# Performance work log

Measured on AMD Instinct MI355X. Metric: run time of the kernel, lower is better.

## Reference

```python
import jax, jax.numpy as jnp
import numpy as np

N_EMBD = 2048
HIDDEN = 2 * N_EMBD        # 4096
ADAPT = HIDDEN // 16       # 256
B, S = 4, 2048


def _layernorm(x, g, b, eps=1e-5):
    mu = jnp.mean(x, axis=-1, keepdims=True)
    var = jnp.var(x, axis=-1, keepdims=True)
    return (x - mu) * jax.lax.rsqrt(var + eps) * g + b


def setup_inputs() -> dict:
    key = jax.random.key(0)
    ks = jax.random.split(key, 7)
    scale = 1.0 / np.sqrt(N_EMBD)
    adapt_scale = scale * 0.01
    return {
        "x": jax.random.normal(ks[0], (B, S, N_EMBD), dtype=jnp.float32),
        "W_up": jax.random.normal(ks[1], (HIDDEN, N_EMBD), dtype=jnp.float32) * scale,
        "W_gate": jax.random.normal(ks[2], (HIDDEN, N_EMBD), dtype=jnp.float32) * scale,
        "W_down": jax.random.normal(ks[3], (N_EMBD, HIDDEN), dtype=jnp.float32) * scale,
        "W_pre": jax.random.normal(ks[4], (ADAPT, N_EMBD), dtype=jnp.float32) * adapt_scale,
        "W_post": jax.random.normal(ks[5], (ADAPT, HIDDEN), dtype=jnp.float32) * adapt_scale,
        "W_proj": jax.random.normal(ks[6], (HIDDEN, ADAPT), dtype=jnp.float32) * adapt_scale,
        "ln_g": jnp.ones((ADAPT,), dtype=jnp.float32),
        "ln_b": jnp.zeros((ADAPT,), dtype=jnp.float32),
    }


def reference(x, W_up, W_gate, W_down, W_pre, W_post, W_proj, ln_g, ln_b):
    # SwiGLU trunk
    up = jnp.einsum('bsd,hd->bsh', x, W_up)
    gate = jnp.einsum('bsd,hd->bsh', x, W_gate)
    hidden = jax.nn.silu(gate) * up                      # [B,S,H]
    # Low-rank quadratic adapter
    adapt_in = _layernorm(jnp.einsum('bsd,ad->bsa', x, W_pre), ln_g, ln_b)       # [B,S,A]
    adapt_out = _layernorm(jnp.einsum('bsh,ah->bsa', hidden, W_post), ln_g, ln_b)  # [B,S,A]
    aw = jnp.einsum('bsa,bta->bst', adapt_in, adapt_out)  # [B,S,S]
    aw = jax.nn.silu(jnp.clip(aw, -5.0, 5.0))
    adapt = jnp.einsum('bst,bta->bsa', aw, adapt_in)      # [B,S,A]
    adapt = 0.1 * jnp.einsum('bsa,ha->bsh', adapt, W_proj)
    hidden = hidden + adapt
    out = jnp.einsum('bsh,dh->bsd', hidden, W_down)       # dropout p=0 -> identity
    return out
```

## Files before the change

### kernel.cpp

```cpp
#include <hip/hip_runtime.h>
#include <cstdint>
#include <cstddef>

typedef unsigned short u16;
typedef short short8 __attribute__((ext_vector_type(8)));
typedef float f32x4 __attribute__((ext_vector_type(4)));

__device__ __forceinline__ u16 f2bf(float f) {
  union { float f; unsigned u; } x; x.f = f;
  unsigned r = x.u + 0x7FFFu + ((x.u >> 16) & 1u);
  return (u16)(r >> 16);
}
__device__ __forceinline__ float b2f(u16 h) {
  union { unsigned u; float f; } x; x.u = ((unsigned)h) << 16;
  return x.f;
}
__device__ __forceinline__ float silu_f(float v) {
  return v / (1.f + __expf(-v));
}
__device__ __forceinline__ void gll(const u16* g, u16* l) {
  __builtin_amdgcn_global_load_lds((const __attribute__((address_space(1))) unsigned*)g,
                                   (__attribute__((address_space(3))) unsigned*)l, 16, 0, 0);
}

__global__ __launch_bounds__(256) void cvt_k(const float4* __restrict__ in,
                                             ushort4* __restrict__ out, int n4) {
  int i = blockIdx.x * 256 + threadIdx.x;
  if (i >= n4) return;
  float4 v = in[i];
  ushort4 o;
  o.x = f2bf(v.x); o.y = f2bf(v.y); o.z = f2bf(v.z); o.w = f2bf(v.w);
  out[i] = o;
}

__global__ __launch_bounds__(256) void red_ln_k(const float* __restrict__ part,
                                                const float* __restrict__ g,
                                                const float* __restrict__ b,
                                                u16* __restrict__ out,
                                                u16* __restrict__ outT, int Mtot) {
  const int row = blockIdx.x;
  const int a = threadIdx.x;
  const size_t stride = (size_t)Mtot * 256;
  const size_t base = (size_t)row * 256 + a;
  float v = part[base] + part[base + stride] + part[base + 2 * stride] + part[base + 3 * stride];
  float s = v, s2 = v * v;
#pragma unroll
  for (int o = 32; o; o >>= 1) { s += __shfl_down(s, o, 64); s2 += __shfl_down(s2, o, 64); }
  __shared__ float red[8];
  int l = a & 63, w = a >> 6;
  if (l == 0) { red[w] = s; red[4 + w] = s2; }
  __syncthreads();
  s  = red[0] + red[1] + red[2] + red[3];
  s2 = red[4] + red[5] + red[6] + red[7];
  float mu  = s * 0.00390625f;
  float var = s2 * 0.00390625f - mu * mu;
  float rs  = rsqrtf(var + 1e-5f);
  float o   = (v - mu) * rs * g[a] + b[a];
  u16 ob = f2bf(o);
  out[base] = ob;
  if (outT) {
    int bi = row >> 11, t = row & 2047;
    outT[((size_t)bi * 256 + a) * 2048 + t] = ob;
  }
}

__global__ __launch_bounds__(256) void red_k(const float* __restrict__ part,
                                             u16* __restrict__ out, int Mtot) {
  const int row = blockIdx.x;
  const int a = threadIdx.x;
  const size_t stride = (size_t)Mtot * 256;
  const size_t base = (size_t)row * 256 + a;
  float v = part[base] + part[base + stride] + part[base + 2 * stride] + part[base + 3 * stride];
  out[base] = f2bf(v);
}

template <int EPI>
__global__ __launch_bounds__(256) void gemm_bt(const u16* __restrict__ A,
                                               const u16* __restrict__ B,
                                               void* __restrict__ Cv,
                                               int M, int N, int K,
                                               long bA, long bB, long bC) {
  __shared__ u16 Al[128 * 64];
  __shared__ u16 Bl[128 * 64];
  const int tid  = threadIdx.x;
  const int bz   = blockIdx.z;
  const int brow = blockIdx.y * 128;
  const int bcol = blockIdx.x * 128;
  A += (size_t)bz * bA;
  B += (size_t)bz * bB;
  const int lane = tid & 63;
  const int w = tid >> 6, wr = w >> 1, wc = w & 1;
  const int srow = tid >> 3;
  const int scol = (tid & 7) * 8;

  f32x4 acc[4][4] = {};

  for (int kt = 0; kt < K; kt += 64) {
#pragma unroll
    for (int i = 0; i < 4; ++i)
      gll(A + (size_t)(brow + i * 32 + srow) * K + kt + scol, &Al[(i * 256 + tid) * 8]);
#pragma unroll
    for (int i = 0; i < 4; ++i)
      gll(B + (size_t)(bcol + i * 32 + srow) * K + kt + scol, &Bl[(i * 256 + tid) * 8]);
    __syncthreads();
#pragma unroll
    for (int kk = 0; kk < 2; ++kk) {
      short8 af[4], bfr[4];
      const int ko = kk * 32 + (lane >> 4) * 8;
#pragma unroll
      for (int m = 0; m < 4; ++m)
        af[m] = *(const short8*)&Al[(wr * 64 + m * 16 + (lane & 15)) * 64 + ko];
#pragma unroll
      for (int n = 0; n < 4; ++n)
        bfr[n] = *(const short8*)&Bl[(wc * 64 + n * 16 + (lane & 15)) * 64 + ko];
#pragma unroll
      for (int m = 0; m < 4; ++m)
#pragma unroll
        for (int n = 0; n < 4; ++n)
          acc[m][n] = __builtin_amdgcn_mfma_f32_16x16x32_bf16(af[m], bfr[n], acc[m][n], 0, 0, 0);
    }
    __syncthreads();
  }

  const int col0 = bcol + wc * 64 + (lane & 15);
  const int row0 = brow + wr * 64 + ((lane >> 4) << 2);
  u16* Cb = (u16*)Cv + (size_t)bz * bC;
#pragma unroll
  for (int m = 0; m < 4; ++m)
#pragma unroll
    for (int j = 0; j < 4; ++j) {
      size_t roff = (size_t)(row0 + m * 16 + j) * N + col0;
#pragma unroll
      for (int n = 0; n < 4; ++n) {
        float v = acc[m][n][j];
        if (EPI == 2) {
          v = fminf(5.f, fmaxf(-5.f, v));
          v = silu_f(v);
        }
        Cb[roff + n * 16] = f2bf(v);
      }
    }
}

__global__ __launch_bounds__(256) void gemm_sk(const u16* __restrict__ A,
                                               const u16* __restrict__ B,
                                               float* __restrict__ part,
                                               int M, int N, int Kfull, int Kc,
                                               long bA, long bB, int Mtot) {
  const int z  = blockIdx.z;
  const int b  = z >> 2, sk = z & 3;
  const int brow = blockIdx.y * 128;
  const int bcol = blockIdx.x * 128;
  A += (size_t)b * bA + (size_t)sk * Kc;
  B += (size_t)b * bB + (size_t)sk * Kc;

  __shared__ u16 Al[128 * 64];
  __shared__ u16 Bl[128 * 64];
  const int tid  = threadIdx.x;
  const int lane = tid & 63;
  const int w = tid >> 6, wr = w >> 1, wc = w & 1;
  const int srow = tid >> 3;
  const int scol = (tid & 7) * 8;

  f32x4 acc[4][4] = {};

  for (int kt = 0; kt < Kc; kt += 64) {
#pragma unroll
    for (int i = 0; i < 4; ++i)
      gll(A + (size_t)(brow + i * 32 + srow) * Kfull + kt + scol, &Al[(i * 256 + tid) * 8]);
#pragma unroll
    for (int i = 0; i < 4; ++i)
      gll(B + (size_t)(bcol + i * 32 + srow) * Kfull + kt + scol, &Bl[(i * 256 + tid) * 8]);
    __syncthreads();
#pragma unroll
    for (int kk = 0; kk < 2; ++kk) {
      short8 af[4], bfr[4];
      const int ko = kk * 32 + (lane >> 4) * 8;
#pragma unroll
      for (int m = 0; m < 4; ++m)
        af[m] = *(const short8*)&Al[(wr * 64 + m * 16 + (lane & 15)) * 64 + ko];
#pragma unroll
      for (int n = 0; n < 4; ++n)
        bfr[n] = *(const short8*)&Bl[(wc * 64 + n * 16 + (lane & 15)) * 64 + ko];
#pragma unroll
      for (int m = 0; m < 4; ++m)
#pragma unroll
        for (int n = 0; n < 4; ++n)
          acc[m][n] = __builtin_amdgcn_mfma_f32_16x16x32_bf16(af[m], bfr[n], acc[m][n], 0, 0, 0);
    }
    __syncthreads();
  }

  const int col0 = bcol + wc * 64 + (lane & 15);
  const int row0 = brow + wr * 64 + ((lane >> 4) << 2);
  float* P = part + ((size_t)sk * Mtot + (size_t)b * M) * N;
#pragma unroll
  for (int m = 0; m < 4; ++m)
#pragma unroll
    for (int j = 0; j < 4; ++j) {
      size_t roff = (size_t)(row0 + m * 16 + j) * N + col0;
#pragma unroll
      for (int n = 0; n < 4; ++n) P[roff + n * 16] = acc[m][n][j];
    }
}

template <int EPI>
__global__ __launch_bounds__(512, 2) void gemm256(const u16* __restrict__ A,
                                                  const u16* __restrict__ B,
                                                  void* __restrict__ Cv,
                                                  const u16* __restrict__ H,
                                                  int M, int N, int K,
                                                  long bA, long bB, long bC) {
  __shared__ __align__(16) u16 As[32768];
  __shared__ __align__(16) u16 Bs[32768];

  const int tid = threadIdx.x;
  const int bz  = blockIdx.z;
  A += (size_t)bz * bA;
  B += (size_t)bz * bB;

  const int gx = gridDim.x;
  const int nwg = gx * gridDim.y;
  int orig = blockIdx.y * gx + blockIdx.x;
  {
    int q = nwg >> 3, r = nwg & 7;
    int xcd = orig & 7, idx = orig >> 3;
    orig = (xcd < r) ? xcd * (q + 1) + idx : r * (q + 1) + (xcd - r) * q + idx;
  }
  const int brow = (orig / gx) * 256;
  const int bcol = (orig % gx) * 256;

  const int lane = tid & 63;
  const int wid  = tid >> 6;
  const int wm = wid >> 2, wn = wid & 3;

  const int srow = tid >> 3;
  const int scol = ((((tid & 7) << 4) ^ ((srow & 7) << 4)) >> 1);
  const u16* Abase = A + (size_t)(brow + srow) * K + scol;
  const u16* Bbase = B + (size_t)(bcol + srow) * K + scol;

  const int fr  = lane & 15;
  const int cs0 = ((((lane >> 4) << 4) ^ ((lane & 7) << 4)) >> 1);
  const int cs1 = cs0 ^ 32;
  const int bro = (wn & 1) * 64;

  const int NT = K >> 6;

  f32x4 acc[8][4] = {};

  {
#pragma unroll
    for (int h = 0; h < 2; ++h) {
      const u16* s = Abase + (size_t)(h * 128) * K;
      u16* d = &As[h * 8192 + tid * 8];
      gll(s, d); gll(s + (size_t)64 * K, d + 4096);
    }
#pragma unroll
    for (int h = 0; h < 2; ++h) {
      const u16* s = Bbase + (size_t)(h * 128) * K;
      u16* d = &Bs[h * 8192 + tid * 8];
      gll(s, d); gll(s + (size_t)64 * K, d + 4096);
    }
  }
  asm volatile("s_waitcnt vmcnt(0)" ::: "memory");
  __builtin_amdgcn_s_barrier();

  for (int t = 0; t < NT; ++t) {
    const int cur = t & 1, nxt = cur ^ 1;
    const bool pf = (t + 1 < NT);
    const int ktn = (t + 1) << 6;
    const u16* aH = &As[(cur * 2 + wm) * 8192];
    const u16* bH = &Bs[(cur * 2 + (wn >> 1)) * 8192];
    short8 af[4], bf[4];

#pragma unroll
    for (int m = 0; m < 4; ++m) af[m] = *(const short8*)(aH + (m * 16 + fr) * 64 + cs0);
#pragma unroll
    for (int n = 0; n < 4; ++n) bf[n] = *(const short8*)(bH + (bro + n * 16 + fr) * 64 + cs0);
    if (pf) {
#pragma unroll
      for (int h = 0; h < 2; ++h) {
        const u16* s = Abase + (size_t)(h * 128) * K + ktn;
        u16* d = &As[(nxt * 2 + h) * 8192 + tid * 8];
        gll(s, d); gll(s + (size_t)64 * K, d + 4096);
      }
    }
    __builtin_amdgcn_s_barrier();
    asm volatile("s_waitcnt lgkmcnt(0)" ::: "memory");
    __builtin_amdgcn_s_setprio(1);
#pragma unroll
    for (int m = 0; m < 4; ++m)
#pragma unroll
      for (int n = 0; n < 4; ++n)
        acc[m][n] = __builtin_amdgcn_mfma_f32_16x16x32_bf16(af[m], bf[n], acc[m][n], 0, 0, 0);
    __builtin_amdgcn_s_setprio(0);
    __builtin_amdgcn_s_barrier();

#pragma unroll
    for (int m = 0; m < 4; ++m) af[m] = *(const short8*)(aH + (64 + m * 16 + fr) * 64 + cs0);
    if (pf) {
#pragma unroll
      for (int h = 0; h < 2; ++h) {
        const u16* s = Bbase + (size_t)(h * 128) * K + ktn;
        u16* d = &Bs[(nxt * 2 + h) * 8192 + tid * 8];
        gll(s, d); gll(s + (size_t)64 * K, d + 4096);
      }
    }
    __builtin_amdgcn_s_barrier();
    asm volatile("s_waitcnt lgkmcnt(0)" ::: "memory");
    __builtin_amdgcn_s_setprio(1);
#pragma unroll
    for (int m = 0; m < 4; ++m)
#pragma unroll
      for (int n = 0; n < 4; ++n)
        acc[4 + m][n] = __builtin_amdgcn_mfma_f32_16x16x32_bf16(af[m], bf[n], acc[4 + m][n], 0, 0, 0);
    __builtin_amdgcn_s_setprio(0);
    __builtin_amdgcn_s_barrier();

#pragma unroll
    for (int m = 0; m < 4; ++m) af[m] = *(const short8*)(aH + (m * 16 + fr) * 64 + cs1);
#pragma unroll
    for (int n = 0; n < 4; ++n) bf[n] = *(const short8*)(bH + (bro + n * 16 + fr) * 64 + cs1);
    __builtin_amdgcn_s_barrier();
    asm volatile("s_waitcnt lgkmcnt(0)" ::: "memory");
    __builtin_amdgcn_s_setprio(1);
#pragma unroll
    for (int m = 0; m < 4; ++m)
#pragma unroll
      for (int n = 0; n < 4; ++n)
        acc[m][n] = __builtin_amdgcn_mfma_f32_16x16x32_bf16(af[m], bf[n], acc[m][n], 0, 0, 0);
    __builtin_amdgcn_s_setprio(0);
    __builtin_amdgcn_s_barrier();

#pragma unroll
    for (int m = 0; m < 4; ++m) af[m] = *(const short8*)(aH + (64 + m * 16 + fr) * 64 + cs1);
    __builtin_amdgcn_s_barrier();
    asm volatile("s_waitcnt lgkmcnt(0)" ::: "memory");
    __builtin_amdgcn_s_setprio(1);
#pragma unroll
    for (int m = 0; m < 4; ++m)
#pragma unroll
      for (int n = 0; n < 4; ++n)
        acc[4 + m][n] = __builtin_amdgcn_mfma_f32_16x16x32_bf16(af[m], bf[n], acc[4 + m][n], 0, 0, 0);
    __builtin_amdgcn_s_setprio(0);
    asm volatile("s_waitcnt vmcnt(0)" ::: "memory");
    __builtin_amdgcn_s_barrier();
  }

  const int col0 = bcol + wn * 64 + fr;
  const int row0 = brow + wm * 128 + ((lane >> 4) << 2);

  if (EPI == 0) {
    float* Cf = (float*)Cv + (size_t)bz * bC;
#pragma unroll
    for (int m = 0; m < 8; ++m)
#pragma unroll
      for (int j = 0; j < 4; ++j) {
        size_t roff = (size_t)(row0 + m * 16 + j) * N + col0;
#pragma unroll
        for (int n = 0; n < 4; ++n) Cf[roff + n * 16] = acc[m][n][j];
      }
  } else if (EPI == 1) {
    u16* Cb = (u16*)Cv + (size_t)bz * bC;
#pragma unroll
    for (int m = 0; m < 8; ++m)
#pragma unroll
      for (int j = 0; j < 4; ++j) {
        size_t roff = (size_t)(row0 + m * 16 + j) * N + col0;
#pragma unroll
        for (int n = 0; n < 4; ++n) Cb[roff + n * 16] = f2bf(acc[m][n][j]);
      }
  } else if (EPI == 2) {
    u16* Cb = (u16*)Cv + (size_t)bz * bC;
#pragma unroll
    for (int m = 0; m < 8; ++m)
#pragma unroll
      for (int j = 0; j < 4; ++j) {
        size_t roff = (size_t)(row0 + m * 16 + j) * N + col0;
#pragma unroll
        for (int n = 0; n < 4; ++n) {
          float v = acc[m][n][j];
          v = fminf(5.f, fmaxf(-5.f, v));
          Cb[roff + n * 16] = f2bf(silu_f(v));
        }
      }
  } else if (EPI == 3) {
    u16* Cb = (u16*)Cv + (size_t)bz * bC;
    const u16* Hb = H + (size_t)bz * bC;
#pragma unroll
    for (int m = 0; m < 8; ++m)
#pragma unroll
      for (int j = 0; j < 4; ++j) {
        size_t roff = (size_t)(row0 + m * 16 + j) * N + col0;
#pragma unroll
        for (int n = 0; n < 4; ++n) {
          size_t idx = roff + n * 16;
          Cb[idx] = f2bf(b2f(Hb[idx]) + 0.1f * acc[m][n][j]);
        }
      }
  } else {
    u16* Cb = (u16*)Cv + (size_t)bz * bC;
    const u16* Hb = H + (size_t)bz * bC;
#pragma unroll
    for (int m = 0; m < 8; ++m)
#pragma unroll
      for (int j = 0; j < 4; ++j) {
        size_t roff = (size_t)(row0 + m * 16 + j) * N + col0;
#pragma unroll
        for (int n = 0; n < 4; ++n) {
          size_t idx = roff + n * 16;
          Cb[idx] = f2bf(silu_f(acc[m][n][j]) * b2f(Hb[idx]));
        }
      }
  }
}

extern "C" void kernel_launch(void* const* d_in, const int* in_sizes, int n_in,
                              void* d_out, int out_size, void* d_ws, size_t ws_size,
                              hipStream_t stream) {
  const float* x      = (const float*)d_in[0];
  const float* W_up   = (const float*)d_in[1];
  const float* W_gate = (const float*)d_in[2];
  const float* W_down = (const float*)d_in[3];
  const float* W_pre  = (const float*)d_in[4];
  const float* W_post = (const float*)d_in[5];
  const float* W_proj = (const float*)d_in[6];
  const float* ln_g   = (const float*)d_in[7];
  const float* ln_b   = (const float*)d_in[8];
  (void)in_sizes; (void)n_in; (void)out_size; (void)ws_size;

  const int D = 2048, Hh = 4096, A_ = 256, Bn = 4, S = 2048, M = 8192;

  char* p = (char*)d_ws;
  u16* xb      = (u16*)p; p += (size_t)M * D * 2;
  u16* Wup_b   = (u16*)p; p += (size_t)Hh * D * 2;
  u16* Wgate_b = (u16*)p; p += (size_t)Hh * D * 2;
  u16* Wdown_b = (u16*)p; p += (size_t)D * Hh * 2;
  u16* Wpre_b  = (u16*)p; p += (size_t)A_ * D * 2;
  u16* Wpost_b = (u16*)p; p += (size_t)A_ * Hh * 2;
  u16* Wproj_b = (u16*)p; p += (size_t)Hh * A_ * 2;
  u16* hidden  = (u16*)p; p += (size_t)M * Hh * 2;
  u16* scratch = (u16*)p; p += (size_t)M * Hh * 2;
  char* q = (char*)scratch;
  u16*   aw        = (u16*)q; q += (size_t)Bn * S * S * 2;
  u16*   adapt_in  = (u16*)q; q += (size_t)M * A_ * 2;
  u16*   adapt_inT = (u16*)q; q += (size_t)M * A_ * 2;
  u16*   adapt_out = (u16*)q; q += (size_t)M * A_ * 2;
  u16*   adaptb    = (u16*)q; q += (size_t)M * A_ * 2;
  float* part = (float*)Wup_b;

  auto cvt = [&](const float* src, u16* dst, size_t n) {
    int n4 = (int)(n / 4);
    cvt_k<<<dim3((n4 + 255) / 256), dim3(256), 0, stream>>>((const float4*)src, (ushort4*)dst, n4);
  };
  cvt(x,      xb,      (size_t)M * D);
  cvt(W_up,   Wup_b,   (size_t)Hh * D);
  cvt(W_gate, Wgate_b, (size_t)Hh * D);
  cvt(W_down, Wdown_b, (size_t)D * Hh);
  cvt(W_pre,  Wpre_b,  (size_t)A_ * D);
  cvt(W_post, Wpost_b, (size_t)A_ * Hh);
  cvt(W_proj, Wproj_b, (size_t)Hh * A_);

  gemm256<1><<<dim3(Hh / 256, M / 256, 1), 512, 0, stream>>>(xb, Wup_b, hidden, nullptr,
                                                             M, Hh, D, 0, 0, 0);
  gemm256<4><<<dim3(Hh / 256, M / 256, 1), 512, 0, stream>>>(xb, Wgate_b, hidden, hidden,
                                                             M, Hh, D, 0, 0, 0);

  gemm_sk<<<dim3(A_ / 128, M / 128, 4), 256, 0, stream>>>(xb, Wpre_b, part,
                                                          M, A_, D, D / 4, 0, 0, M);
  red_ln_k<<<dim3(M), 256, 0, stream>>>(part, ln_g, ln_b, adapt_in, adapt_inT, M);

  gemm_sk<<<dim3(A_ / 128, M / 128, 4), 256, 0, stream>>>(hidden, Wpost_b, part,
                                                          M, A_, Hh, Hh / 4, 0, 0, M);
  red_ln_k<<<dim3(M), 256, 0, stream>>>(part, ln_g, ln_b, adapt_out, nullptr, M);

  gemm_bt<2><<<dim3(S / 128, S / 128, Bn), 256, 0, stream>>>(adapt_in, adapt_out, aw,
                                                             S, S, A_,
                                                             (long)S * A_, (long)S * A_, (long)S * S);

  gemm_sk<<<dim3(A_ / 128, S / 128, Bn * 4), 256, 0, stream>>>(aw, adapt_inT, part,
                                                               S, A_, S, S / 4,
                                                               (long)S * S, (long)A_ * S, M);
  red_k<<<dim3(M), 256, 0, stream>>>(part, adaptb, M);

  gemm256<3><<<dim3(Hh / 256, M / 256, 1), 512, 0, stream>>>(adaptb, Wproj_b, hidden, hidden,
                                                             M, Hh, A_, 0, 0, 0);

  gemm256<0><<<dim3(D / 256, M / 256, 1), 512, 0, stream>>>(hidden, Wdown_b, d_out, nullptr,
                                                            M, D, Hh, 0, 0, 0);
}
```

Baseline: 622.6 us.

## Split gemm256 K-tiles into half-stages with deeper prefetch; fuse seven conversion launches

The 256x256 GEMM now stores each 64-wide K tile as two 32-wide halves with a new XOR swizzle. Loads for the next half-tiles are issued one to two phases ahead, with partial vmcnt waits instead of a full drain each iteration, and the last tiles are handled in a separate tail loop. This aims to hide global-to-LDS latency behind the MFMA work. Separately, the seven fp32-to-bf16 conversion kernels are merged into one launch over the contiguous workspace, using hardcoded offsets that only fit these shapes.

```diff
diff --git a/kernel.cpp b/kernel.cpp
--- a/kernel.cpp
+++ b/kernel.cpp
@@ -23,14 +23,31 @@
                                    (__attribute__((address_space(3))) unsigned*)l, 16, 0, 0);
 }
 
-__global__ __launch_bounds__(256) void cvt_k(const float4* __restrict__ in,
-                                             ushort4* __restrict__ out, int n4) {
-  int i = blockIdx.x * 256 + threadIdx.x;
-  if (i >= n4) return;
-  float4 v = in[i];
+__global__ __launch_bounds__(256) void cvt7_k(const float4* __restrict__ s0,
+                                              const float4* __restrict__ s1,
+                                              const float4* __restrict__ s2,
+                                              const float4* __restrict__ s3,
+                                              const float4* __restrict__ s4,
+                                              const float4* __restrict__ s5,
+                                              const float4* __restrict__ s6,
+                                              ushort4* __restrict__ dst) {
+  const int i = blockIdx.x * 256 + threadIdx.x;
+  const int o1 = 4194304, o2 = 6291456, o3 = 8388608, o4 = 10485760,
+            o5 = 10616832, o6 = 10878976, o7 = 11141120;
+  if (i >= o7) return;
+  const float4* src;
+  int base;
+  if      (i < o1) { src = s0; base = 0;  }
+  else if (i < o2) { src = s1; base = o1; }
+  else if (i < o3) { src = s2; base = o2; }
+  else if (i < o4) { src = s3; base = o3; }
+  else if (i < o5) { src = s4; base = o4; }
+  else if (i < o6) { src = s5; base = o5; }
+  else             { src = s6; base = o6; }
+  float4 v = src[i - base];
   ushort4 o;
   o.x = f2bf(v.x); o.y = f2bf(v.y); o.z = f2bf(v.z); o.w = f2bf(v.w);
-  out[i] = o;
+  dst[i] = o;
 }
 
 __global__ __launch_bounds__(256) void red_ln_k(const float* __restrict__ part,
@@ -234,118 +251,125 @@
   const int wid  = tid >> 6;
   const int wm = wid >> 2, wn = wid & 3;
 
-  const int srow = tid >> 3;
-  const int scol = ((((tid & 7) << 4) ^ ((srow & 7) << 4)) >> 1);
-  const u16* Abase = A + (size_t)(brow + srow) * K + scol;
-  const u16* Bbase = B + (size_t)(bcol + srow) * K + scol;
+  const int srow   = tid >> 2;
+  const int schunk = (((tid & 3) ^ ((tid >> 3) & 3)) << 3);
+  const u16* Asrc = A + (size_t)(brow + srow) * K + schunk;
+  const u16* Bsrc = B + (size_t)(bcol + srow) * K + schunk;
+  const int sdst = tid * 8;
 
   const int fr  = lane & 15;
-  const int cs0 = ((((lane >> 4) << 4) ^ ((lane & 7) << 4)) >> 1);
-  const int cs1 = cs0 ^ 32;
-  const int bro = (wn & 1) * 64;
+  const int rc8 = (((lane >> 4) ^ ((lane >> 1) & 3)) << 3);
+  const int aoff0 = (wm * 128 + fr) * 32 + rc8;
+  const int boff0 = (wn * 64 + fr) * 32 + rc8;
 
   const int NT = K >> 6;
-
   f32x4 acc[8][4] = {};
 
-  {
-#pragma unroll
-    for (int h = 0; h < 2; ++h) {
-      const u16* s = Abase + (size_t)(h * 128) * K;
-      u16* d = &As[h * 8192 + tid * 8];
-      gll(s, d); gll(s + (size_t)64 * K, d + 4096);
-    }
-#pragma unroll
-    for (int h = 0; h < 2; ++h) {
-      const u16* s = Bbase + (size_t)(h * 128) * K;
-      u16* d = &Bs[h * 8192 + tid * 8];
-      gll(s, d); gll(s + (size_t)64 * K, d + 4096);
-    }
-  }
-  asm volatile("s_waitcnt vmcnt(0)" ::: "memory");
+  auto stA = [&](int tt, int kq) {
+    u16* d = &As[(((tt & 1) * 2 + kq) << 13) + sdst];
+    const u16* s = Asrc + (size_t)(tt << 6) + kq * 32;
+    gll(s, d); gll(s + (size_t)128 * K, d + 4096);
+  };
+  auto stB = [&](int tt, int kq) {
+    u16* d = &Bs[(((tt & 1) * 2 + kq) << 13) + sdst];
+    const u16* s = Bsrc + (size_t)(tt << 6) + kq * 32;
+    gll(s, d); gll(s + (size_t)128 * K, d + 4096);
+  };
+
+  stA(0, 0); stB(0, 0); stA(0, 1); stB(0, 1); stA(1, 0); stB(1, 0);
+  asm volatile("s_waitcnt vmcnt(8)" ::: "memory");
   __builtin_amdgcn_s_barrier();
 
-  for (int t = 0; t < NT; ++t) {
-    const int cur = t & 1, nxt = cur ^ 1;
-    const bool pf = (t + 1 < NT);
-    const int ktn = (t + 1) << 6;
-    const u16* aH = &As[(cur * 2 + wm) * 8192];
-    const u16* bH = &Bs[(cur * 2 + (wn >> 1)) * 8192];
+#define PH_READ_A(kqbase, mlo)                                                   \
+  {                                                                              \
+    _Pragma("unroll")                                                            \
+    for (int m = 0; m < 4; ++m)                                                  \
+      af[m] = *(const short8*)(kqbase + aoff0 + (mlo + m) * 512);                \
+  }
+#define PH_READ_B(kqbase)                                                        \
+  {                                                                              \
+    _Pragma("unroll")                                                            \
+    for (int n = 0; n < 4; ++n)                                                  \
+      bf[n] = *(const short8*)(kqbase + boff0 + n * 512);                        \
+  }
+#define PH_MFMA(mlo)                                                             \
+  __builtin_amdgcn_s_barrier();                                                  \
+  asm volatile("s_waitcnt lgkmcnt(0)" ::: "memory");                             \
+  __builtin_amdgcn_s_setprio(1);                                                 \
+  {                                                                              \
+    _Pragma("unroll")                                                            \
+    for (int m = 0; m < 4; ++m)                                                  \
+      _Pragma("unroll")                                                          \
+      for (int n = 0; n < 4; ++n)                                                \
+        acc[mlo + m][n] =                                                        \
+            __builtin_amdgcn_mfma_f32_16x16x32_bf16(af[m], bf[n], acc[mlo + m][n], 0, 0, 0); \
+  }                                                                              \
+  __builtin_amdgcn_s_setprio(0);
+
+  int t = 0;
+  for (; t < NT - 3; ++t) {
+    const int cur = t & 1;
+    const u16* a0 = &As[(cur * 2) << 13];
+    const u16* b0 = &Bs[(cur * 2) << 13];
+    const u16* a1 = a0 + 8192;
+    const u16* b1 = b0 + 8192;
     short8 af[4], bf[4];
 
-#pragma unroll
-    for (int m = 0; m < 4; ++m) af[m] = *(const short8*)(aH + (m * 16 + fr) * 64 + cs0);
-#pragma unroll
-    for (int n = 0; n < 4; ++n) bf[n] = *(const short8*)(bH + (bro + n * 16 + fr) * 64 + cs0);
-    if (pf) {
-#pragma unroll
-      for (int h = 0; h < 2; ++h) {
-        const u16* s = Abase + (size_t)(h * 128) * K + ktn;
-        u16* d = &As[(nxt * 2 + h) * 8192 + tid * 8];
-        gll(s, d); gll(s + (size_t)64 * K, d + 4096);
-      }
-    }
-    __builtin_amdgcn_s_barrier();
-    asm volatile("s_waitcnt lgkmcnt(0)" ::: "memory");
-    __builtin_amdgcn_s_setprio(1);
-#pragma unroll
-    for (int m = 0; m < 4; ++m)
-#pragma unroll
-      for (int n = 0; n < 4; ++n)
-        acc[m][n] = __builtin_amdgcn_mfma_f32_16x16x32_bf16(af[m], bf[n], acc[m][n], 0, 0, 0);
-    __builtin_amdgcn_s_setprio(0);
-    __builtin_amdgcn_s_barrier();
-
-#pragma unroll
-    for (int m = 0; m < 4; ++m) af[m] = *(const short8*)(aH + (64 + m * 16 + fr) * 64 + cs0);
-    if (pf) {
-#pragma unroll
-      for (int h = 0; h < 2; ++h) {
-        const u16* s = Bbase + (size_t)(h * 128) * K + ktn;
-        u16* d = &Bs[(nxt * 2 + h) * 8192 + tid * 8];
-        gll(s, d); gll(s + (size_t)64 * K, d + 4096);
-      }
-    }
-    __builtin_amdgcn_s_barrier();
-    asm volatile("s_waitcnt lgkmcnt(0)" ::: "memory");
-    __builtin_amdgcn_s_setprio(1);
-#pragma unroll
-    for (int m = 0; m < 4; ++m)
-#pragma unroll
-      for (int n = 0; n < 4; ++n)
-        acc[4 + m][n] = __builtin_amdgcn_mfma_f32_16x16x32_bf16(af[m], bf[n], acc[4 + m][n], 0, 0, 0);
-    __builtin_amdgcn_s_setprio(0);
-    __builtin_amdgcn_s_barrier();
-
-#pragma unroll
-    for (int m = 0; m < 4; ++m) af[m] = *(const short8*)(aH + (m * 16 + fr) * 64 + cs1);
-#pragma unroll
-    for (int n = 0; n < 4; ++n) bf[n] = *(const short8*)(bH + (bro + n * 16 + fr) * 64 + cs1);
-    __builtin_amdgcn_s_barrier();
-    asm volatile("s_waitcnt lgkmcnt(0)" ::: "memory");
-    __builtin_amdgcn_s_setprio(1);
-#pragma unroll
-    for (int m = 0; m < 4; ++m)
-#pragma unroll
-      for (int n = 0; n < 4; ++n)
-        acc[m][n] = __builtin_amdgcn_mfma_f32_16x16x32_bf16(af[m], bf[n], acc[m][n], 0, 0, 0);
-    __builtin_amdgcn_s_setprio(0);
-    __builtin_amdgcn_s_barrier();
-
-#pragma unroll
-    for (int m = 0; m < 4; ++m) af[m] = *(const short8*)(aH + (64 + m * 16 + fr) * 64 + cs1);
-    __builtin_amdgcn_s_barrier();
-    asm volatile("s_waitcnt lgkmcnt(0)" ::: "memory");
-    __builtin_amdgcn_s_setprio(1);
-#pragma unroll
-    for (int m = 0; m < 4; ++m)
-#pragma unroll
-      for (int n = 0; n < 4; ++n)
-        acc[4 + m][n] = __builtin_amdgcn_mfma_f32_16x16x32_bf16(af[m], bf[n], acc[4 + m][n], 0, 0, 0);
-    __builtin_amdgcn_s_setprio(0);
+    PH_READ_A(a0, 0) PH_READ_B(b0)
+    stA(t + 1, 1);
+    PH_MFMA(0)
+    __builtin_amdgcn_s_barrier();
+
+    PH_READ_A(a0, 4)
+    stB(t + 1, 1);
+    PH_MFMA(4)
+    asm volatile("s_waitcnt vmcnt(8)" ::: "memory");
+    __builtin_amdgcn_s_barrier();
+
+    PH_READ_A(a1, 0) PH_READ_B(b1)
+    stA(t + 2, 0);
+    PH_MFMA(0)
+    __builtin_amdgcn_s_barrier();
+
+    PH_READ_A(a1, 4)
+    stB(t + 2, 0);
+    PH_MFMA(4)
+    asm volatile("s_waitcnt vmcnt(8)" ::: "memory");
+    __builtin_amdgcn_s_barrier();
+  }
+  for (; t < NT; ++t) {
+    const int cur = t & 1;
+    const u16* a0 = &As[(cur * 2) << 13];
+    const u16* b0 = &Bs[(cur * 2) << 13];
+    const u16* a1 = a0 + 8192;
+    const u16* b1 = b0 + 8192;
+    short8 af[4], bf[4];
+
+    PH_READ_A(a0, 0) PH_READ_B(b0)
+    if (t + 1 < NT) stA(t + 1, 1);
+    PH_MFMA(0)
+    __builtin_amdgcn_s_barrier();
+
+    PH_READ_A(a0, 4)
+    if (t + 1 < NT) stB(t + 1, 1);
+    PH_MFMA(4)
     asm volatile("s_waitcnt vmcnt(0)" ::: "memory");
     __builtin_amdgcn_s_barrier();
-  }
+
+    PH_READ_A(a1, 0) PH_READ_B(b1)
+    if (t + 2 < NT) stA(t + 2, 0);
+    PH_MFMA(0)
+    __builtin_amdgcn_s_barrier();
+
+    PH_READ_A(a1, 4)
+    if (t + 2 < NT) stB(t + 2, 0);
+    PH_MFMA(4)
+    asm volatile("s_waitcnt vmcnt(0)" ::: "memory");
+    __builtin_amdgcn_s_barrier();
+  }
+#undef PH_READ_A
+#undef PH_READ_B
+#undef PH_MFMA
 
   const int col0 = bcol + wn * 64 + fr;
   const int row0 = brow + wm * 128 + ((lane >> 4) << 2);
@@ -449,17 +473,10 @@
   u16*   adaptb    = (u16*)q; q += (size_t)M * A_ * 2;
   float* part = (float*)Wup_b;
 
-  auto cvt = [&](const float* src, u16* dst, size_t n) {
-    int n4 = (int)(n / 4);
-    cvt_k<<<dim3((n4 + 255) / 256), dim3(256), 0, stream>>>((const float4*)src, (ushort4*)dst, n4);
-  };
-  cvt(x,      xb,      (size_t)M * D);
-  cvt(W_up,   Wup_b,   (size_t)Hh * D);
-  cvt(W_gate, Wgate_b, (size_t)Hh * D);
-  cvt(W_down, Wdown_b, (size_t)D * Hh);
-  cvt(W_pre,  Wpre_b,  (size_t)A_ * D);
-  cvt(W_post, Wpost_b, (size_t)A_ * Hh);
-  cvt(W_proj, Wproj_b, (size_t)Hh * A_);
+  cvt7_k<<<dim3(43520), dim3(256), 0, stream>>>((const float4*)x, (const float4*)W_up,
+                                                (const float4*)W_gate, (const float4*)W_down,
+                                                (const float4*)W_pre, (const float4*)W_post,
+                                                (const float4*)W_proj, (ushort4*)xb);
 
   gemm256<1><<<dim3(Hh / 256, M / 256, 1), 512, 0, stream>>>(xb, Wup_b, hidden, nullptr,
                                                              M, Hh, D, 0, 0, 0);
```

After: 635.6 us. 2.1% more time.
